# Optimization experiments

Hardware: AMD Instinct MI355X
Metric: run time of the kernel (lower is better)

## Reference

```python
import jax, jax.numpy as jnp
import numpy as np

C = 512
NUM_HEADS = 8
HEAD_DIM = C // NUM_HEADS
GROUPS = 32
EPS = 1e-5


def setup_inputs() -> dict:
    key = jax.random.key(0)
    ks = jax.random.split(key, 7)
    N, H, W = 16, 32, 32
    x = jax.random.normal(ks[0], (N, C, H, W), dtype=jnp.float32)
    norm_w = jax.random.normal(ks[1], (C,), dtype=jnp.float32) * 0.02 + 1.0
    norm_b = jax.random.normal(ks[2], (C,), dtype=jnp.float32) * 0.02
    qkv_w = jax.random.normal(ks[3], (3 * C, C), dtype=jnp.float32) * (1.0 / np.sqrt(C))
    qkv_b = jax.random.normal(ks[4], (3 * C,), dtype=jnp.float32) * 0.02
    proj_w = jax.random.normal(ks[5], (C, C), dtype=jnp.float32) * (1.0 / np.sqrt(C))
    proj_b = jax.random.normal(ks[6], (C,), dtype=jnp.float32) * 0.02
    return {"x": x, "norm_w": norm_w, "norm_b": norm_b, "qkv_w": qkv_w,
            "qkv_b": qkv_b, "proj_w": proj_w, "proj_b": proj_b}


def _group_norm(x, w, b):
    N, Cc, H, W = x.shape
    xg = x.reshape(N, GROUPS, Cc // GROUPS, H, W)
    mean = xg.mean(axis=(2, 3, 4), keepdims=True)
    var = xg.var(axis=(2, 3, 4), keepdims=True)
    xg = (xg - mean) * jax.lax.rsqrt(var + EPS)
    return xg.reshape(N, Cc, H, W) * w[None, :, None, None] + b[None, :, None, None]


def reference(x, norm_w, norm_b, qkv_w, qkv_b, proj_w, proj_b):
    N, Cc, H, W = x.shape
    S = H * W
    h = _group_norm(x, norm_w, norm_b)
    # 1x1 conv == per-pixel linear over channels
    qkv = jnp.einsum('nchw,oc->nohw', h, qkv_w) + qkv_b[None, :, None, None]
    q, k, v = jnp.split(qkv, 3, axis=1)  # each [N, C, H, W]
    # [N, heads, head_dim, S]
    q = q.reshape(N, NUM_HEADS, HEAD_DIM, S)
    k = k.reshape(N, NUM_HEADS, HEAD_DIM, S)
    v = v.reshape(N, NUM_HEADS, HEAD_DIM, S)
    scale = HEAD_DIM ** -0.5
    attn = jnp.einsum('nhds,nhdt->nhst', q, k) * scale  # [N,heads,S,S]
    attn = jax.nn.softmax(attn, axis=-1)
    out = jnp.einsum('nhst,nhdt->nhds', attn, v)  # [N,heads,head_dim,S]
    out = out.reshape(N, Cc, H, W)
    out = jnp.einsum('nchw,oc->nohw', out, proj_w) + proj_b[None, :, None, None]
    return out + x
```

## Files before the change

### kernel.cpp

```cpp
#include <hip/hip_runtime.h>
#include <cstdint>
#include <cstddef>

typedef unsigned short u16;
typedef __attribute__((ext_vector_type(8))) short bf16x8;
typedef __attribute__((ext_vector_type(4))) short bf16x4;
typedef __attribute__((ext_vector_type(4))) float f32x4;
typedef __attribute__((ext_vector_type(16))) float f32x16;
typedef __attribute__((ext_vector_type(4))) unsigned short u16x4;

#define NB 16
#define CD 512
#define SD 1024
#define NH 8
#define HD 64

#define QSCL 0.18033688011112042f

__device__ __forceinline__ u16 f2bf(float f) {
    unsigned u = __float_as_uint(f);
    u += 0x7FFF + ((u >> 16) & 1);
    return (u16)(u >> 16);
}
__device__ __forceinline__ unsigned cvt_pk(float lo, float hi) {
    unsigned r;
    asm("v_cvt_pk_bf16_f32 %0, %1, %2" : "=v"(r) : "v"(lo), "v"(hi));
    return r;
}
__device__ __forceinline__ float exp2v(float x) {
    float r;
    asm("v_exp_f32 %0, %1" : "=v"(r) : "v"(x));
    return r;
}
__device__ __forceinline__ void gload16(const void* g, void* l) {
    __builtin_amdgcn_global_load_lds(
        (const __attribute__((address_space(1))) void*)g,
        (__attribute__((address_space(3))) void*)l, 16, 0, 0);
}

__global__ __launch_bounds__(256) void cvt2_kernel(
    const float* __restrict__ s0, u16* __restrict__ d0,
    const float* __restrict__ s1, u16* __restrict__ d1)
{
    const int bid = blockIdx.x;
    const float* s;
    u16* d;
    int i;
    if (bid < 768) { s = s0; d = d0; i = (bid * 256 + threadIdx.x) * 4; }
    else           { s = s1; d = d1; i = ((bid - 768) * 256 + threadIdx.x) * 4; }
    float4 v = *reinterpret_cast<const float4*>(s + i);
    u16x4 o = { f2bf(v.x), f2bf(v.y), f2bf(v.z), f2bf(v.w) };
    *reinterpret_cast<u16x4*>(d + i) = o;
}

__global__ __launch_bounds__(256) void gn_kernel(
    const float* __restrict__ x, const float* __restrict__ w,
    const float* __restrict__ b, u16* __restrict__ h)
{
    const int n = blockIdx.x >> 5, g = blockIdx.x & 31;
    const size_t base = ((size_t)n * CD + g * 16) * SD;
    const float4* xp = reinterpret_cast<const float4*>(x + base);

    float4 vals[16];
    float sum = 0.f, ss = 0.f;
#pragma unroll
    for (int i = 0; i < 16; ++i) {
        float4 v = xp[threadIdx.x + (i << 8)];
        vals[i] = v;
        sum += v.x + v.y + v.z + v.w;
        ss  += v.x*v.x + v.y*v.y + v.z*v.z + v.w*v.w;
    }
#pragma unroll
    for (int off = 32; off > 0; off >>= 1) {
        sum += __shfl_down(sum, off);
        ss  += __shfl_down(ss,  off);
    }
    __shared__ float rs[4], rq[4];
    const int wid = threadIdx.x >> 6, lane = threadIdx.x & 63;
    if (lane == 0) { rs[wid] = sum; rq[wid] = ss; }
    __syncthreads();
    const float tsum = rs[0] + rs[1] + rs[2] + rs[3];
    const float tss  = rq[0] + rq[1] + rq[2] + rq[3];
    const float mean = tsum * (1.0f / 16384.0f);
    const float var  = tss * (1.0f / 16384.0f) - mean * mean;
    const float inv  = rsqrtf(var + 1e-5f);

    u16* hp = h + ((size_t)n * SD + 4 * threadIdx.x) * CD + g * 16;
#pragma unroll
    for (int i = 0; i < 16; ++i) {
        const float A  = inv * w[g * 16 + i];
        const float Bc = b[g * 16 + i] - mean * A;
        float4 v = vals[i];
        hp[i]          = f2bf(v.x * A + Bc);
        hp[CD + i]     = f2bf(v.y * A + Bc);
        hp[2 * CD + i] = f2bf(v.z * A + Bc);
        hp[3 * CD + i] = f2bf(v.w * A + Bc);
    }
}

template<int MODE>
__global__ __launch_bounds__(256) void mfma_gemm(
    const u16* __restrict__ Wb, const u16* __restrict__ act,
    const float* __restrict__ bias, const float* __restrict__ resid,
    void* __restrict__ outp, u16* __restrict__ vtout, int M)
{
    const int nb = blockIdx.z, m0 = blockIdx.y * 128, s0 = blockIdx.x * 128;
    __shared__ u16 Al[128 * 64];
    __shared__ u16 Bl[128 * 64];
    const int tid = threadIdx.x, wv = tid >> 6, ln = tid & 63;
    const int wm = wv >> 1, wn = wv & 1, lr = ln & 15, lg = ln >> 4;

    const f32x4 zero = {0.f, 0.f, 0.f, 0.f};
    f32x4 acc[4][4];
#pragma unroll
    for (int i = 0; i < 4; ++i)
#pragma unroll
        for (int j = 0; j < 4; ++j) acc[i][j] = zero;

    const u16* Ab = Wb + (size_t)m0 * CD;
    const u16* Bb = act + ((size_t)nb * SD + s0) * CD;

    for (int k0 = 0; k0 < CD; k0 += 64) {
        __syncthreads();
#pragma unroll
        for (int r = 0; r < 4; ++r) {
            const int gi = (r * 4 + wv) * 64 + ln;
            const int row = gi >> 3, gc = gi & 7;
            const int sg = ((gc ^ (row & 7)) * 8);
            gload16(Ab + (size_t)row * CD + k0 + sg, Al + gi * 8);
            gload16(Bb + (size_t)row * CD + k0 + sg, Bl + gi * 8);
        }
        __syncthreads();

#pragma unroll
        for (int kc = 0; kc < 2; ++kc) {
            bf16x8 af[4], bfr[4];
#pragma unroll
            for (int mi = 0; mi < 4; ++mi) {
                const int row = wm * 64 + mi * 16 + lr;
                af[mi] = *reinterpret_cast<const bf16x8*>(
                    Al + row * 64 + (((kc * 4 + lg) ^ (row & 7)) * 8));
            }
#pragma unroll
            for (int nj = 0; nj < 4; ++nj) {
                const int row = wn * 64 + nj * 16 + lr;
                bfr[nj] = *reinterpret_cast<const bf16x8*>(
                    Bl + row * 64 + (((kc * 4 + lg) ^ (row & 7)) * 8));
            }
#pragma unroll
            for (int mi = 0; mi < 4; ++mi)
#pragma unroll
                for (int nj = 0; nj < 4; ++nj) {
                    if (MODE == 0)
                        acc[mi][nj] = __builtin_amdgcn_mfma_f32_16x16x32_bf16(
                            af[mi], bfr[nj], acc[mi][nj], 0, 0, 0);
                    else
                        acc[mi][nj] = __builtin_amdgcn_mfma_f32_16x16x32_bf16(
                            bfr[mi], af[nj], acc[mi][nj], 0, 0, 0);
                }
        }
    }

    if (MODE == 0) {
        if (m0 < 1024) {
            u16* o = (u16*)outp;
            const float sc = (m0 < 512) ? QSCL : 1.0f;
#pragma unroll
            for (int mi = 0; mi < 4; ++mi) {
                const int mb = m0 + wm * 64 + mi * 16 + lg * 4;
#pragma unroll
                for (int nj = 0; nj < 4; ++nj) {
                    const int s = s0 + wn * 64 + nj * 16 + lr;
                    u16x4 pack;
#pragma unroll
                    for (int r = 0; r < 4; ++r)
                        pack[r] = f2bf((acc[mi][nj][r] + bias[mb + r]) * sc);
                    *reinterpret_cast<u16x4*>(o + ((size_t)nb * SD + s) * 1024 + mb) = pack;
                }
            }
        } else {
#pragma unroll
            for (int mi = 0; mi < 4; ++mi)
#pragma unroll
                for (int r = 0; r < 4; ++r) {
                    const int m = m0 + wm * 64 + mi * 16 + lg * 4 + r;
                    const float bi = bias[m];
#pragma unroll
                    for (int nj = 0; nj < 4; ++nj) {
                        const int s = s0 + wn * 64 + nj * 16 + lr;
                        vtout[((size_t)nb * 512 + (m - 1024)) * SD + s] = f2bf(acc[mi][nj][r] + bi);
                    }
                }
        }
    } else {
        float* o = (float*)outp;
#pragma unroll
        for (int i = 0; i < 4; ++i)
#pragma unroll
            for (int j = 0; j < 4; ++j) {
                const int m = m0 + wm * 64 + j * 16 + lr;
                const int s = s0 + wn * 64 + i * 16 + lg * 4;
                const float bi = bias[m];
                const size_t idx = ((size_t)nb * M + m) * SD + s;
                float4 r4 = *reinterpret_cast<const float4*>(resid + idx);
                float4 v;
                v.x = acc[i][j][0] + bi + r4.x;
                v.y = acc[i][j][1] + bi + r4.y;
                v.z = acc[i][j][2] + bi + r4.z;
                v.w = acc[i][j][3] + bi + r4.w;
                *reinterpret_cast<float4*>(o + idx) = v;
            }
    }
}

__global__ __launch_bounds__(512) void attn_mfma(
    const u16* __restrict__ qk, const u16* __restrict__ vt, u16* __restrict__ ao)
{
    const int nh = blockIdx.y, n = nh >> 3, hh = nh & 7;
    const int q0 = blockIdx.x << 8;
    const int tid = threadIdx.x, wv = tid >> 6, ln = tid & 63;
    const int lq = ln & 31, hi = ln >> 5;

    __shared__ u16 Kl[2][64 * 64];
    __shared__ u16 Vl[2][64 * 64];

    const u16* Qb = qk + (size_t)n * SD * 1024 + hh * HD;
    const u16* Kb = Qb + 512;
    const u16* Vb = vt + ((size_t)n * 512 + hh * HD) * SD;

    bf16x8 qf[4];
    {
        const u16* qp = Qb + (size_t)(q0 + wv * 32 + lq) * 1024 + hi * 8;
#pragma unroll
        for (int ks = 0; ks < 4; ++ks)
            qf[ks] = *reinterpret_cast<const bf16x8*>(qp + ks * 16);
    }

    f32x16 of0 = {}, of1 = {};
    float mrun = -INFINITY, lrun = 0.f;

    const int srow = tid >> 3, sgc = tid & 7;
    const int ssw = (sgc ^ (srow & 7)) * 8;
    const u16* Ksrc = Kb + (size_t)srow * 1024 + ssw;
    const u16* Vsrc = Vb + (size_t)srow * SD + ssw;

    gload16(Ksrc, &Kl[0][tid * 8]);
    gload16(Vsrc, &Vl[0][tid * 8]);
    __syncthreads();

    int cur = 0;
    for (int tt = 0; tt < 16; ++tt) {
        if (tt < 15) {
            const int t1 = (tt + 1) << 6;
            gload16(Ksrc + (size_t)t1 * 1024, &Kl[cur ^ 1][tid * 8]);
            gload16(Vsrc + t1, &Vl[cur ^ 1][tid * 8]);
        }
        f32x16 st0 = {}, st1 = {};
        const u16* Kc = &Kl[cur][0];
        __builtin_amdgcn_s_setprio(1);
#pragma unroll
        for (int ks = 0; ks < 4; ++ks) {
            const int g = (((ks * 2 + hi) ^ (lq & 7)) * 8);
            bf16x8 k0 = *reinterpret_cast<const bf16x8*>(Kc + lq * 64 + g);
            bf16x8 k1 = *reinterpret_cast<const bf16x8*>(Kc + (32 + lq) * 64 + g);
            st0 = __builtin_amdgcn_mfma_f32_32x32x16_bf16(k0, qf[ks], st0, 0, 0, 0);
            st1 = __builtin_amdgcn_mfma_f32_32x32x16_bf16(k1, qf[ks], st1, 0, 0, 0);
        }
        __builtin_amdgcn_s_setprio(0);
        float mx = st0[0];
#pragma unroll
        for (int r = 1; r < 16; ++r) mx = fmaxf(mx, st0[r]);
#pragma unroll
        for (int r = 0; r < 16; ++r) mx = fmaxf(mx, st1[r]);
        mx = fmaxf(mx, __shfl_xor(mx, 32));
        if (!__all(mx - mrun <= 8.0f)) {
            const float mn = fmaxf(mrun, mx);
            const float al = exp2v(mrun - mn);
            mrun = mn;
            lrun *= al;
#pragma unroll
            for (int r = 0; r < 16; ++r) { of0[r] *= al; of1[r] *= al; }
        }
        float ps = 0.f;
        float p0[16], p1[16];
#pragma unroll
        for (int r = 0; r < 16; ++r) { p0[r] = exp2v(st0[r] - mrun); ps += p0[r]; }
#pragma unroll
        for (int r = 0; r < 16; ++r) { p1[r] = exp2v(st1[r] - mrun); ps += p1[r]; }
        ps += __shfl_xor(ps, 32);
        lrun += ps;

        const u16* Vc = &Vl[cur][0];
        __builtin_amdgcn_s_setprio(1);
#pragma unroll
        for (int ks = 0; ks < 4; ++ks) {
            union { unsigned w[4]; bf16x8 v; } pf;
            const int rb = (ks & 1) * 8;
            if (ks < 2) {
                pf.w[0] = cvt_pk(p0[rb + 0], p0[rb + 1]);
                pf.w[1] = cvt_pk(p0[rb + 2], p0[rb + 3]);
                pf.w[2] = cvt_pk(p0[rb + 4], p0[rb + 5]);
                pf.w[3] = cvt_pk(p0[rb + 6], p0[rb + 7]);
            } else {
                pf.w[0] = cvt_pk(p1[rb + 0], p1[rb + 1]);
                pf.w[1] = cvt_pk(p1[rb + 2], p1[rb + 3]);
                pf.w[2] = cvt_pk(p1[rb + 4], p1[rb + 5]);
                pf.w[3] = cvt_pk(p1[rb + 6], p1[rb + 7]);
            }
            const int e0 = ((2 * ks) ^ (lq & 7)) * 8 + hi * 4;
            const int e1 = ((2 * ks + 1) ^ (lq & 7)) * 8 + hi * 4;
            union { bf16x4 h[2]; bf16x8 v; } vf0, vf1;
            vf0.h[0] = *reinterpret_cast<const bf16x4*>(Vc + lq * 64 + e0);
            vf0.h[1] = *reinterpret_cast<const bf16x4*>(Vc + lq * 64 + e1);
            vf1.h[0] = *reinterpret_cast<const bf16x4*>(Vc + (32 + lq) * 64 + e0);
            vf1.h[1] = *reinterpret_cast<const bf16x4*>(Vc + (32 + lq) * 64 + e1);
            of0 = __builtin_amdgcn_mfma_f32_32x32x16_bf16(vf0.v, pf.v, of0, 0, 0, 0);
            of1 = __builtin_amdgcn_mfma_f32_32x32x16_bf16(vf1.v, pf.v, of1, 0, 0, 0);
        }
        __builtin_amdgcn_s_setprio(0);
        __syncthreads();
        cur ^= 1;
    }

    const float inv = 1.0f / lrun;
    u16* op = ao + ((size_t)n * SD + q0 + wv * 32 + lq) * CD + hh * HD;
#pragma unroll
    for (int g = 0; g < 4; ++g) {
        u16x4 o0, o1;
#pragma unroll
        for (int e = 0; e < 4; ++e) {
            o0[e] = f2bf(of0[g * 4 + e] * inv);
            o1[e] = f2bf(of1[g * 4 + e] * inv);
        }
        const int d0 = g * 8 + hi * 4;
        *reinterpret_cast<u16x4*>(op + d0) = o0;
        *reinterpret_cast<u16x4*>(op + 32 + d0) = o1;
    }
}

extern "C" void kernel_launch(void* const* d_in, const int* in_sizes, int n_in,
                              void* d_out, int out_size, void* d_ws, size_t ws_size,
                              hipStream_t stream)
{
    const float* x      = (const float*)d_in[0];
    const float* norm_w = (const float*)d_in[1];
    const float* norm_b = (const float*)d_in[2];
    const float* qkv_w  = (const float*)d_in[3];
    const float* qkv_b  = (const float*)d_in[4];
    const float* proj_w = (const float*)d_in[5];
    const float* proj_b = (const float*)d_in[6];

    u16* h   = (u16*)d_ws;
    u16* qkb = h + (size_t)NB * SD * CD;
    u16* vtb = qkb + (size_t)NB * SD * 1024;
    u16* ao  = vtb + (size_t)NB * 512 * SD;
    u16* wq  = ao + (size_t)NB * SD * CD;
    u16* wp  = wq + (size_t)1536 * CD;

    hipLaunchKernelGGL(cvt2_kernel, dim3(1024), dim3(256), 0, stream,
                       qkv_w, wq, proj_w, wp);
    hipLaunchKernelGGL(gn_kernel, dim3(NB * 32), dim3(256), 0, stream, x, norm_w, norm_b, h);
    hipLaunchKernelGGL((mfma_gemm<0>), dim3(8, 12, NB), dim3(256), 0, stream,
                       wq, h, qkv_b, (const float*)nullptr, (void*)qkb, vtb, 1536);
    hipLaunchKernelGGL(attn_mfma, dim3(SD / 256, NB * NH), dim3(512), 0, stream,
                       qkb, vtb, ao);
    hipLaunchKernelGGL((mfma_gemm<1>), dim3(8, 4, NB), dim3(256), 0, stream,
                       wp, ao, proj_b, x, (void*)d_out, (u16*)nullptr, 512);
}
```

Measured before the change: 219.5 us.

## Shrink attention blocks to 128 queries, swizzle V layout, tree-reduce softmax

The attention kernel now uses 256-thread blocks covering 128 queries instead of 512 threads covering 256. The grid is reordered so consecutive blocks share query position across heads, and each thread loads two K/V chunks per tile. The V transpose written by the QKV GEMM gets an XOR swizzle on the sequence index, matched by a new read key in attention, to cut LDS bank conflicts on the half-row V reads. The softmax max and sum become tree reductions with multiple accumulators, and the probabilities are stored in the score registers to shorten dependency chains and free registers. Smaller blocks give more of them and possibly higher occupancy, but K/V tiles are reloaded twice as often per query.

```diff
diff --git a/kernel.cpp b/kernel.cpp
--- a/kernel.cpp
+++ b/kernel.cpp
@@ -179,6 +179,7 @@
                 }
             }
         } else {
+            const int sswap = (lg >= 2) ? 4 : 0;
 #pragma unroll
             for (int mi = 0; mi < 4; ++mi)
 #pragma unroll
@@ -187,7 +188,7 @@
                     const float bi = bias[m];
 #pragma unroll
                     for (int nj = 0; nj < 4; ++nj) {
-                        const int s = s0 + wn * 64 + nj * 16 + lr;
+                        const int s = (s0 + wn * 64 + nj * 16 + lr) ^ sswap;
                         vtout[((size_t)nb * 512 + (m - 1024)) * SD + s] = f2bf(acc[mi][nj][r] + bi);
                     }
                 }
@@ -213,11 +214,11 @@
     }
 }
 
-__global__ __launch_bounds__(512) void attn_mfma(
+__global__ __launch_bounds__(256) void attn_mfma(
     const u16* __restrict__ qk, const u16* __restrict__ vt, u16* __restrict__ ao)
 {
-    const int nh = blockIdx.y, n = nh >> 3, hh = nh & 7;
-    const int q0 = blockIdx.x << 8;
+    const int nh = blockIdx.x, n = nh >> 3, hh = nh & 7;
+    const int q0 = blockIdx.y << 7;
     const int tid = threadIdx.x, wv = tid >> 6, ln = tid & 63;
     const int lq = ln & 31, hi = ln >> 5;
 
@@ -239,21 +240,27 @@
     f32x16 of0 = {}, of1 = {};
     float mrun = -INFINITY, lrun = 0.f;
 
-    const int srow = tid >> 3, sgc = tid & 7;
-    const int ssw = (sgc ^ (srow & 7)) * 8;
-    const u16* Ksrc = Kb + (size_t)srow * 1024 + ssw;
-    const u16* Vsrc = Vb + (size_t)srow * SD + ssw;
-
-    gload16(Ksrc, &Kl[0][tid * 8]);
-    gload16(Vsrc, &Vl[0][tid * 8]);
+    const int i0 = tid, i1 = tid + 256;
+    const int sr0 = i0 >> 3, g0 = ((i0 & 7) ^ (sr0 & 7)) * 8;
+    const int sr1 = i1 >> 3, g1 = ((i1 & 7) ^ (sr1 & 7)) * 8;
+    const u16* Ks0 = Kb + (size_t)sr0 * 1024 + g0;
+    const u16* Ks1 = Kb + (size_t)sr1 * 1024 + g1;
+    const u16* Vs0 = Vb + (size_t)sr0 * SD + g0;
+    const u16* Vs1 = Vb + (size_t)sr1 * SD + g1;
+
+    gload16(Ks0, &Kl[0][i0 * 8]);  gload16(Ks1, &Kl[0][i1 * 8]);
+    gload16(Vs0, &Vl[0][i0 * 8]);  gload16(Vs1, &Vl[0][i1 * 8]);
     __syncthreads();
 
+    const int hkey = (hi ^ ((lq >> 3) & 1)) * 4;
     int cur = 0;
     for (int tt = 0; tt < 16; ++tt) {
         if (tt < 15) {
             const int t1 = (tt + 1) << 6;
-            gload16(Ksrc + (size_t)t1 * 1024, &Kl[cur ^ 1][tid * 8]);
-            gload16(Vsrc + t1, &Vl[cur ^ 1][tid * 8]);
+            gload16(Ks0 + (size_t)t1 * 1024, &Kl[cur ^ 1][i0 * 8]);
+            gload16(Ks1 + (size_t)t1 * 1024, &Kl[cur ^ 1][i1 * 8]);
+            gload16(Vs0 + t1, &Vl[cur ^ 1][i0 * 8]);
+            gload16(Vs1 + t1, &Vl[cur ^ 1][i1 * 8]);
         }
         f32x16 st0 = {}, st1 = {};
         const u16* Kc = &Kl[cur][0];
@@ -267,11 +274,12 @@
             st1 = __builtin_amdgcn_mfma_f32_32x32x16_bf16(k1, qf[ks], st1, 0, 0, 0);
         }
         __builtin_amdgcn_s_setprio(0);
-        float mx = st0[0];
-#pragma unroll
-        for (int r = 1; r < 16; ++r) mx = fmaxf(mx, st0[r]);
-#pragma unroll
-        for (int r = 0; r < 16; ++r) mx = fmaxf(mx, st1[r]);
+        float tm[8];
+#pragma unroll
+        for (int i = 0; i < 8; ++i)
+            tm[i] = fmaxf(fmaxf(st0[i], st0[i + 8]), fmaxf(st1[i], st1[i + 8]));
+        float mx = fmaxf(fmaxf(fmaxf(tm[0], tm[1]), fmaxf(tm[2], tm[3])),
+                         fmaxf(fmaxf(tm[4], tm[5]), fmaxf(tm[6], tm[7])));
         mx = fmaxf(mx, __shfl_xor(mx, 32));
         if (!__all(mx - mrun <= 8.0f)) {
             const float mn = fmaxf(mrun, mx);
@@ -281,12 +289,22 @@
 #pragma unroll
             for (int r = 0; r < 16; ++r) { of0[r] *= al; of1[r] *= al; }
         }
-        float ps = 0.f;
-        float p0[16], p1[16];
-#pragma unroll
-        for (int r = 0; r < 16; ++r) { p0[r] = exp2v(st0[r] - mrun); ps += p0[r]; }
-#pragma unroll
-        for (int r = 0; r < 16; ++r) { p1[r] = exp2v(st1[r] - mrun); ps += p1[r]; }
+        float sa = 0.f, sb = 0.f, sc = 0.f, sd = 0.f;
+#pragma unroll
+        for (int r = 0; r < 16; r += 4) {
+            st0[r]     = exp2v(st0[r]     - mrun); sa += st0[r];
+            st0[r + 1] = exp2v(st0[r + 1] - mrun); sb += st0[r + 1];
+            st0[r + 2] = exp2v(st0[r + 2] - mrun); sc += st0[r + 2];
+            st0[r + 3] = exp2v(st0[r + 3] - mrun); sd += st0[r + 3];
+        }
+#pragma unroll
+        for (int r = 0; r < 16; r += 4) {
+            st1[r]     = exp2v(st1[r]     - mrun); sa += st1[r];
+            st1[r + 1] = exp2v(st1[r + 1] - mrun); sb += st1[r + 1];
+            st1[r + 2] = exp2v(st1[r + 2] - mrun); sc += st1[r + 2];
+            st1[r + 3] = exp2v(st1[r + 3] - mrun); sd += st1[r + 3];
+        }
+        float ps = (sa + sb) + (sc + sd);
         ps += __shfl_xor(ps, 32);
         lrun += ps;
 
@@ -297,18 +315,18 @@
             union { unsigned w[4]; bf16x8 v; } pf;
             const int rb = (ks & 1) * 8;
             if (ks < 2) {
-                pf.w[0] = cvt_pk(p0[rb + 0], p0[rb + 1]);
-                pf.w[1] = cvt_pk(p0[rb + 2], p0[rb + 3]);
-                pf.w[2] = cvt_pk(p0[rb + 4], p0[rb + 5]);
-                pf.w[3] = cvt_pk(p0[rb + 6], p0[rb + 7]);
+                pf.w[0] = cvt_pk(st0[rb + 0], st0[rb + 1]);
+                pf.w[1] = cvt_pk(st0[rb + 2], st0[rb + 3]);
+                pf.w[2] = cvt_pk(st0[rb + 4], st0[rb + 5]);
+                pf.w[3] = cvt_pk(st0[rb + 6], st0[rb + 7]);
             } else {
-                pf.w[0] = cvt_pk(p1[rb + 0], p1[rb + 1]);
-                pf.w[1] = cvt_pk(p1[rb + 2], p1[rb + 3]);
-                pf.w[2] = cvt_pk(p1[rb + 4], p1[rb + 5]);
-                pf.w[3] = cvt_pk(p1[rb + 6], p1[rb + 7]);
-            }
-            const int e0 = ((2 * ks) ^ (lq & 7)) * 8 + hi * 4;
-            const int e1 = ((2 * ks + 1) ^ (lq & 7)) * 8 + hi * 4;
+                pf.w[0] = cvt_pk(st1[rb + 0], st1[rb + 1]);
+                pf.w[1] = cvt_pk(st1[rb + 2], st1[rb + 3]);
+                pf.w[2] = cvt_pk(st1[rb + 4], st1[rb + 5]);
+                pf.w[3] = cvt_pk(st1[rb + 6], st1[rb + 7]);
+            }
+            const int e0 = ((2 * ks) ^ (lq & 7)) * 8 + hkey;
+            const int e1 = ((2 * ks + 1) ^ (lq & 7)) * 8 + hkey;
             union { bf16x4 h[2]; bf16x8 v; } vf0, vf1;
             vf0.h[0] = *reinterpret_cast<const bf16x4*>(Vc + lq * 64 + e0);
             vf0.h[1] = *reinterpret_cast<const bf16x4*>(Vc + lq * 64 + e1);
@@ -362,7 +380,7 @@
     hipLaunchKernelGGL(gn_kernel, dim3(NB * 32), dim3(256), 0, stream, x, norm_w, norm_b, h);
     hipLaunchKernelGGL((mfma_gemm<0>), dim3(8, 12, NB), dim3(256), 0, stream,
                        wq, h, qkv_b, (const float*)nullptr, (void*)qkb, vtb, 1536);
-    hipLaunchKernelGGL(attn_mfma, dim3(SD / 256, NB * NH), dim3(512), 0, stream,
+    hipLaunchKernelGGL(attn_mfma, dim3(NB * NH, SD / 128), dim3(256), 0, stream,
                        qkb, vtb, ao);
     hipLaunchKernelGGL((mfma_gemm<1>), dim3(8, 4, NB), dim3(256), 0, stream,
                        wp, ao, proj_b, x, (void*)d_out, (u16*)nullptr, 512);
```

Measured after the change: 248.6 us. 1.13x slower.
